# Optimization experiments

Hardware: AMD Instinct MI355X
Metric: run time of the kernel (lower is better)

The kernel has to match this reference:

```python
import jax, jax.numpy as jnp
import numpy as np

VOCAB = 9
D = 128      # EMBED_DIM
S = 64       # SEQ_LEN / context_length
B = 512      # batch
NH = 4       # num_heads
DH = D // NH # head dim = 32
NB = 2       # num_blocks
EPS = 1e-5


def setup_inputs() -> dict:
    key = jax.random.key(0)
    ks = jax.random.split(key, 10)
    rn = lambda k, shape: jax.random.normal(k, shape, jnp.float32) * 0.02
    return {
        "x": jax.random.randint(ks[0], (B, S), 0, VOCAB),
        "emb": rn(ks[1], (VOCAB, D)),
        "ln1_w": jnp.ones((NB, D), jnp.float32),          # pre-sLSTM LayerNorm weight
        "Wg": rn(ks[2], (NB, 4, NH, DH, DH)),             # headwise gate projections (i,f,z,o)
        "R": rn(ks[3], (NB, NH, DH, 4 * DH)),             # recurrent kernels per head
        "bias": rn(ks[4], (NB, NH, 4, DH)),               # cell bias per head/gate
        "gn_w": jnp.ones((NB, D), jnp.float32),           # multi-head (group) norm weight
        "ln2_w": jnp.ones((NB, D), jnp.float32),          # pre-FF LayerNorm weight
        "ff_up_w": rn(ks[5], (NB, 2 * D, D)),             # gated FF up projection
        "ff_down_w": rn(ks[6], (NB, D, D)),               # FF down projection
        "post_w": jnp.ones((D,), jnp.float32),            # post-blocks LayerNorm weight
        "proj_w": rn(ks[7], (VOCAB, D)),
        "proj_b": jnp.zeros((VOCAB,), jnp.float32),
    }


def _layernorm(x, w):
    mu = x.mean(-1, keepdims=True)
    var = x.var(-1, keepdims=True)
    return (x - mu) * jax.lax.rsqrt(var + EPS) * w


def _mh_groupnorm(h, w):
    # h: [B,S,NH,DH] -> normalize over DH per head, scale by per-channel w [D]
    mu = h.mean(-1, keepdims=True)
    var = h.var(-1, keepdims=True)
    hn = (h - mu) * jax.lax.rsqrt(var + EPS)
    return hn.reshape(h.shape[0], h.shape[1], D) * w


def _slstm_layer(xh, Wg, R, b):
    # xh: [B,S,NH,DH]; Wg: [4,NH,DH,DH]; R: [NH,DH,4*DH]; b: [NH,4,DH]
    gx = jnp.einsum('bsnh,gnkh->sbngk', xh, Wg)  # [S,B,NH,4,DH] gate preacts (i,f,z,o)

    def step(carry, g):
        h, c, n, m = carry  # each [B,NH,DH]
        ry = jnp.einsum('bnh,nhk->bnk', h, R).reshape(h.shape[0], NH, 4, DH)
        raw = g + ry + b
        i_r, f_r, z_r, o_r = raw[:, :, 0], raw[:, :, 1], raw[:, :, 2], raw[:, :, 3]
        logfplusm = m + jax.nn.log_sigmoid(f_r)
        mnew = jnp.maximum(i_r, logfplusm)            # stabilizer
        ig = jnp.exp(i_r - mnew)
        fg = jnp.exp(logfplusm - mnew)
        cnew = fg * c + ig * jnp.tanh(z_r)
        nnew = fg * n + ig
        hnew = jax.nn.sigmoid(o_r) * cnew / nnew
        return (hnew, cnew, nnew, mnew), hnew

    z0 = jnp.zeros((xh.shape[0], NH, DH), xh.dtype)
    _, hs = jax.lax.scan(step, (z0, z0, z0, z0), gx)
    return hs.transpose(1, 0, 2, 3)  # [B,S,NH,DH]


def reference(x, emb, ln1_w, Wg, R, bias, gn_w, ln2_w, ff_up_w, ff_down_w, post_w, proj_w, proj_b):
    h = emb[x]  # [B,S,D]
    for bi in range(NB):
        xn = _layernorm(h, ln1_w[bi])
        y = _slstm_layer(xn.reshape(h.shape[0], S, NH, DH), Wg[bi], R[bi], bias[bi])
        h = h + _mh_groupnorm(y, gn_w[bi])
        xn = _layernorm(h, ln2_w[bi])
        up = xn @ ff_up_w[bi].T                       # [B,S,2D]
        gate, upv = up[..., :D], up[..., D:]
        h = h + (jax.nn.gelu(gate, approximate=False) * upv) @ ff_down_w[bi].T
    h = _layernorm(h, post_w)
    return h @ proj_w.T + proj_b  # [B,S,VOCAB]
```

## Files before the change

### kernel.cpp

```cpp
#include <hip/hip_runtime.h>
#include <math.h>

#define D      128
#define S_LEN  64
#define B_SZ   512
#define NH     4
#define DH     32
#define NB     2
#define VOCAB  9
#define EPS    1e-5f
#define NTOK   (B_SZ * S_LEN)

template <int CTRL>
__device__ __forceinline__ float dppf(float x) {
    return __int_as_float(__builtin_amdgcn_update_dpp(
        0, __float_as_int(x), CTRL, 0xF, 0xF, true));
}
__device__ __forceinline__ float wsum64(float x) {
    x += dppf<0x111>(x);
    x += dppf<0x112>(x);
    x += dppf<0x114>(x);
    x += dppf<0x118>(x);
    x += dppf<0x142>(x);
    x += dppf<0x143>(x);
    return __int_as_float(__builtin_amdgcn_readlane(__float_as_int(x), 63));
}

__device__ __forceinline__ int xc3(int t, int c) { return c ^ (((t >> 1) & 7) << 2); }
__device__ __forceinline__ int xa (int t, int c) { return c ^ ((t & 7) << 2); }
__device__ __forceinline__ int xg (int c)        { return c ^ ((c >> 5) << 3); }

__global__ __launch_bounds__(256) void k_embed(const int* __restrict__ x,
                                               const float* __restrict__ emb,
                                               float* __restrict__ h,
                                               float* __restrict__ stats)
{
    int lane = threadIdx.x & 63;
    int wv   = threadIdx.x >> 6;
    int tok  = blockIdx.x * 4 + wv;
    int xi   = x[tok];
    float2 v = ((const float2*)(emb + xi * D))[lane];
    ((float2*)(h + (size_t)tok * D))[lane] = v;
    float s1 = wsum64(v.x + v.y);
    float s2 = wsum64(v.x * v.x + v.y * v.y);
    float mu  = s1 * (1.0f / D);
    float var = s2 * (1.0f / D) - mu * mu;
    if (lane == 0) {
        stats[tok * 2]     = mu;
        stats[tok * 2 + 1] = rsqrtf(var + EPS);
    }
}

__global__ __launch_bounds__(256, 2) void k_gx(const float* __restrict__ Wg,
                                               const float* __restrict__ bias,
                                               const float* __restrict__ lnw,
                                               const float* __restrict__ h,
                                               const float* __restrict__ stats,
                                               float* __restrict__ gx)
{
    __shared__ float xs[32 * 128];
    __shared__ float wl[4 * 32 * 128];

    int tid  = threadIdx.x;
    int lane = tid & 63;
    int wv   = tid >> 6;
    size_t tok0 = (size_t)blockIdx.x * 32;

    {
        int q = tid & 7;
        #pragma unroll
        for (int it = 0; it < 16; ++it) {
            int row = it * 32 + (tid >> 3);
            int g  = row >> 7;
            int n  = (row >> 5) & 3;
            int hh = row & 31;
            float4 v = *(const float4*)(Wg + row * 32 + q * 4);
            int col = g * 32 + hh;
            int sw  = q << 2;
            float* dst = wl + n * 4096;
            dst[(q * 4 + 0) * 128 + (col ^ sw)] = v.x;
            dst[(q * 4 + 1) * 128 + (col ^ sw)] = v.y;
            dst[(q * 4 + 2) * 128 + (col ^ sw)] = v.z;
            dst[(q * 4 + 3) * 128 + (col ^ sw)] = v.w;
        }
    }
    for (int i = 0; i < 8; ++i) {
        int t = wv * 8 + i;
        const float* hp = h + (tok0 + t) * D;
        float mu = stats[(tok0 + t) * 2];
        float rs = stats[(tok0 + t) * 2 + 1];
        float v1 = (hp[lane]      - mu) * rs * lnw[lane];
        float v2 = (hp[64 + lane] - mu) * rs * lnw[64 + lane];
        xs[t * 128 + xg(lane)]      = v1;
        xs[t * 128 + xg(lane + 64)] = v2;
    }
    __syncthreads();

    int nh   = lane >> 4;
    int col0 = (lane & 15) * 8;
    int t0   = wv * 8;

    float acc[8][8];
    #pragma unroll
    for (int j = 0; j < 8; ++j)
        #pragma unroll
        for (int cc = 0; cc < 8; ++cc) acc[j][cc] = 0.f;

    const float* wbase = wl + nh * 4096;
    #pragma unroll
    for (int k4 = 0; k4 < 8; ++k4) {
        int sw  = k4 << 2;
        int ac4 = (nh * 32 + k4 * 4) ^ (nh << 3);
        float4 w0[4], w1[4];
        #pragma unroll
        for (int i = 0; i < 4; ++i) {
            int k = k4 * 4 + i;
            w0[i] = *(const float4*)&wbase[k * 128 + (col0 ^ sw)];
            w1[i] = *(const float4*)&wbase[k * 128 + ((col0 + 4) ^ sw)];
        }
        #pragma unroll
        for (int j = 0; j < 8; ++j) {
            float4 a4 = *(const float4*)&xs[(t0 + j) * 128 + ac4];
            #pragma unroll
            for (int i = 0; i < 4; ++i) {
                float a = ((const float*)&a4)[i];
                acc[j][0] = fmaf(a, w0[i].x, acc[j][0]);
                acc[j][1] = fmaf(a, w0[i].y, acc[j][1]);
                acc[j][2] = fmaf(a, w0[i].z, acc[j][2]);
                acc[j][3] = fmaf(a, w0[i].w, acc[j][3]);
                acc[j][4] = fmaf(a, w1[i].x, acc[j][4]);
                acc[j][5] = fmaf(a, w1[i].y, acc[j][5]);
                acc[j][6] = fmaf(a, w1[i].z, acc[j][6]);
                acc[j][7] = fmaf(a, w1[i].w, acc[j][7]);
            }
        }
    }

    float4 bb0 = *(const float4*)(bias + nh * 128 + col0);
    float4 bb1 = *(const float4*)(bias + nh * 128 + col0 + 4);
    #pragma unroll
    for (int j = 0; j < 8; ++j) {
        int gt = (int)tok0 + t0 + j;
        int bb = gt >> 6;
        int ss = gt & 63;
        float* op = gx + ((size_t)(bb * NH + nh) * S_LEN + ss) * 128 + col0;
        float4 o0v, o1v;
        o0v.x = acc[j][0] + bb0.x; o0v.y = acc[j][1] + bb0.y;
        o0v.z = acc[j][2] + bb0.z; o0v.w = acc[j][3] + bb0.w;
        o1v.x = acc[j][4] + bb1.x; o1v.y = acc[j][5] + bb1.y;
        o1v.z = acc[j][6] + bb1.z; o1v.w = acc[j][7] + bb1.w;
        *(float4*)op       = o0v;
        *(float4*)(op + 4) = o1v;
    }
}

__global__ __launch_bounds__(64, 2) void k_scan(const float* __restrict__ Rm,
                                                const float* __restrict__ gnw,
                                                const float* __restrict__ gx,
                                                float* __restrict__ h)
{
    __shared__ float WA[8][64][4];
    __shared__ float WB[8][64][4];

    int b    = blockIdx.x >> 2;
    int n    = blockIdx.x & 3;
    int lane = threadIdx.x;
    int e    = lane >> 1;
    int sub  = lane & 1;
    int colA = sub * DH + e;

    #pragma unroll
    for (int cc = 0; cc < 8; ++cc) {
        float4 a, bv;
        #pragma unroll
        for (int j = 0; j < 4; ++j) {
            ((float*)&a)[j]  = Rm[(n * DH + cc * 4 + j) * 128 + colA];
            ((float*)&bv)[j] = Rm[(n * DH + cc * 4 + j) * 128 + 64 + colA];
        }
        *(float4*)WA[cc][lane] = a;
        *(float4*)WB[cc][lane] = bv;
    }
    float gw = gnw[n * DH + e];
    __syncthreads();

    float c = 0.f, nacc = 0.f, m = 0.f;
    float hu[DH];
    #pragma unroll
    for (int i = 0; i < DH; ++i) hu[i] = 0.f;

    float* hb = h + ((size_t)b * S_LEN) * D + n * DH;
    const float* gxp = gx + ((size_t)(b * NH + n) * S_LEN) * 128;

    float pGA[4], pGB[4], pHR[4];
    #pragma unroll
    for (int k = 0; k < 4; ++k) {
        pGA[k] = gxp[k * 128 + colA];
        pGB[k] = gxp[k * 128 + 64 + colA];
        pHR[k] = hb[k * D + e];
    }

    #pragma unroll 4
    for (int s = 0; s < S_LEN; ++s) {
        int sp = (s + 4 < S_LEN) ? s + 4 : S_LEN - 1;
        float nGA = gxp[sp * 128 + colA];
        float nGB = gxp[sp * 128 + 64 + colA];
        float nHR = hb[sp * D + e];

        float r0=0,r1=0,r2=0,r3=0,q0=0,q1=0,q2=0,q3=0;
        #pragma unroll
        for (int cc = 0; cc < 8; ++cc) {
            float4 wa = *(const float4*)WA[cc][lane];
            float4 wb = *(const float4*)WB[cc][lane];
            r0 = fmaf(hu[cc*4+0], wa.x, r0);
            r1 = fmaf(hu[cc*4+1], wa.y, r1);
            r2 = fmaf(hu[cc*4+2], wa.z, r2);
            r3 = fmaf(hu[cc*4+3], wa.w, r3);
            q0 = fmaf(hu[cc*4+0], wb.x, q0);
            q1 = fmaf(hu[cc*4+1], wb.y, q1);
            q2 = fmaf(hu[cc*4+2], wb.z, q2);
            q3 = fmaf(hu[cc*4+3], wb.w, q3);
        }
        float rawA = pGA[0] + ((r0 + r1) + (r2 + r3));
        float rawB = pGB[0] + ((q0 + q1) + (q2 + q3));

        float xA = dppf<0xB1>(rawA);
        float xB = dppf<0xB1>(rawB);
        float i_r = sub ? xA   : rawA;
        float f_r = sub ? rawA : xA;
        float z_r = sub ? xB   : rawB;
        float o_r = sub ? rawB : xB;

        float lsf  = fminf(f_r, 0.f)
                   - 0.69314718055994531f * __log2f(1.0f + __expf(-fabsf(f_r)));
        float lfm  = m + lsf;
        float mnew = fmaxf(i_r, lfm);
        float ig   = __expf(i_r - mnew);
        float fg   = __expf(lfm - mnew);
        float t    = __expf(2.f * z_r);
        float tz   = 1.f - 2.f / (t + 1.f);
        c    = fg * c + ig * tz;
        nacc = fg * nacc + ig;
        m    = mnew;
        float hv = c / (nacc * (1.f + __expf(-o_r)));

        float s1 = wsum64(hv);
        float s2 = wsum64(hv * hv);
        float mu  = s1 * (1.f / 64.f);
        float var = s2 * (1.f / 64.f) - mu * mu;
        float hn  = (hv - mu) * rsqrtf(var + EPS) * gw;

        if (!sub) hb[s * D + e] = pHR[0] + hn;

        #pragma unroll
        for (int i = 0; i < DH; ++i)
            hu[i] = __int_as_float(
                __builtin_amdgcn_readlane(__float_as_int(hv), 2 * i));

        pGA[0]=pGA[1]; pGA[1]=pGA[2]; pGA[2]=pGA[3]; pGA[3]=nGA;
        pGB[0]=pGB[1]; pGB[1]=pGB[2]; pGB[2]=pGB[3]; pGB[3]=nGB;
        pHR[0]=pHR[1]; pHR[1]=pHR[2]; pHR[2]=pHR[3]; pHR[3]=nHR;
    }
}

template <int LAST>
__global__ __launch_bounds__(256, 3) void k_ff(float* __restrict__ h,
                                               const float* __restrict__ ln2w,
                                               const float* __restrict__ wup,
                                               const float* __restrict__ wdn,
                                               float* __restrict__ stats_out,
                                               const float* __restrict__ lastw,
                                               const float* __restrict__ projw,
                                               const float* __restrict__ projb,
                                               float* __restrict__ out)
{
    __shared__ float xs[32 * 128];
    __shared__ float as_[32 * 64];
    __shared__ float wt[2 * 32 * 64];

    int tid  = threadIdx.x;
    int lane = tid & 63;
    int wv   = tid >> 6;
    size_t tok0 = (size_t)blockIdx.x * 32;

    for (int i = 0; i < 8; ++i) {
        int t = wv * 8 + i;
        const float* hp = h + (tok0 + t) * D;
        float v1 = hp[lane], v2 = hp[64 + lane];
        float s1 = wsum64(v1 + v2);
        float s2 = wsum64(v1 * v1 + v2 * v2);
        float mu = s1 * (1.0f / D);
        float rs = rsqrtf(s2 * (1.0f / D) - mu * mu + EPS);
        xs[t * D + xc3(t, lane)]      = (v1 - mu) * rs * ln2w[lane];
        xs[t * D + xc3(t, lane + 64)] = (v2 - mu) * rs * ln2w[64 + lane];
    }

    int q     = tid & 7;
    int r0    = tid >> 3;
    int goff0 = r0 * D + q * 4;
    int goff1 = (r0 + 32) * D + q * 4;
    int s0    = r0 ^ (q << 2);
    int kb    = q * 4;

    auto ffld = [&](int id, float4* pre) {
        int p = (id >= 6) ? 1 : 0;
        int j = id - p * 6;
        const float* b0;
        const float* b1;
        if (j < 4) { b0 = wup + (p * 64) * D + j * 32;
                     b1 = wup + (128 + p * 64) * D + j * 32; }
        else       { int jj = j - 4;
                     b0 = wdn + p * 64 + jj * 32;
                     b1 = wdn + 64 * D + p * 64 + jj * 32; }
        pre[0] = *(const float4*)(b0 + goff0);
        pre[1] = *(const float4*)(b0 + goff1);
        pre[2] = *(const float4*)(b1 + goff0);
        pre[3] = *(const float4*)(b1 + goff1);
    };
    auto fst = [&](const float4* pre) {
        #pragma unroll
        for (int cc = 0; cc < 4; ++cc) {
            const float* p0 = (const float*)&pre[0];
            const float* p1 = (const float*)&pre[1];
            const float* p2 = (const float*)&pre[2];
            const float* p3 = (const float*)&pre[3];
            wt[(kb + cc) * 64 + s0]           = p0[cc];
            wt[(kb + cc) * 64 + s0 + 32]      = p1[cc];
            wt[2048 + (kb + cc) * 64 + s0]      = p2[cc];
            wt[2048 + (kb + cc) * 64 + s0 + 32] = p3[cc];
        }
    };

    int ti = tid >> 4;
    int oi = tid & 15;
    int t0 = ti * 2;
    int o0 = oi * 4;

    float accd[2][2][4];
    #pragma unroll
    for (int a1 = 0; a1 < 2; ++a1)
        #pragma unroll
        for (int j = 0; j < 2; ++j)
            #pragma unroll
            for (int cc = 0; cc < 4; ++cc) accd[a1][j][cc] = 0.f;

    float4 pre[4];
    ffld(0, pre);
    int id = 1;

    #pragma unroll
    for (int p = 0; p < 2; ++p) {
        float accg[2][4], accv[2][4];
        #pragma unroll
        for (int j = 0; j < 2; ++j)
            #pragma unroll
            for (int cc = 0; cc < 4; ++cc) { accg[j][cc] = 0.f; accv[j][cc] = 0.f; }

        for (int c4 = 0; c4 < 4; ++c4) {
            __syncthreads();
            fst(pre);
            if (id < 12) ffld(id, pre);
            ++id;
            __syncthreads();
            int kc = c4 * 32;
            #pragma unroll
            for (int k4 = 0; k4 < 8; ++k4) {
                float4 a0 = *(const float4*)&xs[t0 * D + xc3(t0, kc + k4 * 4)];
                float4 a1v = *(const float4*)&xs[(t0 + 1) * D + xc3(t0 + 1, kc + k4 * 4)];
                int ws = k4 << 2;
                #pragma unroll
                for (int i = 0; i < 4; ++i) {
                    int k = k4 * 4 + i;
                    float4 bg = *(const float4*)&wt[k * 64 + (o0 ^ ws)];
                    float4 bv = *(const float4*)&wt[2048 + k * 64 + (o0 ^ ws)];
                    float ax0 = ((const float*)&a0)[i];
                    float ax1 = ((const float*)&a1v)[i];
                    accg[0][0] = fmaf(ax0, bg.x, accg[0][0]);
                    accg[0][1] = fmaf(ax0, bg.y, accg[0][1]);
                    accg[0][2] = fmaf(ax0, bg.z, accg[0][2]);
                    accg[0][3] = fmaf(ax0, bg.w, accg[0][3]);
                    accg[1][0] = fmaf(ax1, bg.x, accg[1][0]);
                    accg[1][1] = fmaf(ax1, bg.y, accg[1][1]);
                    accg[1][2] = fmaf(ax1, bg.z, accg[1][2]);
                    accg[1][3] = fmaf(ax1, bg.w, accg[1][3]);
                    accv[0][0] = fmaf(ax0, bv.x, accv[0][0]);
                    accv[0][1] = fmaf(ax0, bv.y, accv[0][1]);
                    accv[0][2] = fmaf(ax0, bv.z, accv[0][2]);
                    accv[0][3] = fmaf(ax0, bv.w, accv[0][3]);
                    accv[1][0] = fmaf(ax1, bv.x, accv[1][0]);
                    accv[1][1] = fmaf(ax1, bv.y, accv[1][1]);
                    accv[1][2] = fmaf(ax1, bv.z, accv[1][2]);
                    accv[1][3] = fmaf(ax1, bv.w, accv[1][3]);
                }
            }
        }
        #pragma unroll
        for (int j = 0; j < 2; ++j) {
            int t = t0 + j;
            float4 av;
            float* ap = (float*)&av;
            #pragma unroll
            for (int cc = 0; cc < 4; ++cc) {
                float g = accg[j][cc];
                float u = accv[j][cc];
                ap[cc] = 0.5f * g * (1.0f + erff(g * 0.70710678118654752f)) * u;
            }
            *(float4*)&as_[t * 64 + xa(t, o0)] = av;
        }
        for (int c2 = 0; c2 < 2; ++c2) {
            __syncthreads();
            fst(pre);
            if (id < 12) ffld(id, pre);
            ++id;
            __syncthreads();
            int kc = c2 * 32;
            #pragma unroll
            for (int k4 = 0; k4 < 8; ++k4) {
                float4 a0 = *(const float4*)&as_[t0 * 64 + xa(t0, kc + k4 * 4)];
                float4 a1v = *(const float4*)&as_[(t0 + 1) * 64 + xa(t0 + 1, kc + k4 * 4)];
                int ws = k4 << 2;
                #pragma unroll
                for (int i = 0; i < 4; ++i) {
                    int k = k4 * 4 + i;
                    float4 b0v = *(const float4*)&wt[k * 64 + (o0 ^ ws)];
                    float4 b1v = *(const float4*)&wt[2048 + k * 64 + (o0 ^ ws)];
                    float ax0 = ((const float*)&a0)[i];
                    float ax1 = ((const float*)&a1v)[i];
                    accd[0][0][0] = fmaf(ax0, b0v.x, accd[0][0][0]);
                    accd[0][0][1] = fmaf(ax0, b0v.y, accd[0][0][1]);
                    accd[0][0][2] = fmaf(ax0, b0v.z, accd[0][0][2]);
                    accd[0][0][3] = fmaf(ax0, b0v.w, accd[0][0][3]);
                    accd[0][1][0] = fmaf(ax1, b0v.x, accd[0][1][0]);
                    accd[0][1][1] = fmaf(ax1, b0v.y, accd[0][1][1]);
                    accd[0][1][2] = fmaf(ax1, b0v.z, accd[0][1][2]);
                    accd[0][1][3] = fmaf(ax1, b0v.w, accd[0][1][3]);
                    accd[1][0][0] = fmaf(ax0, b1v.x, accd[1][0][0]);
                    accd[1][0][1] = fmaf(ax0, b1v.y, accd[1][0][1]);
                    accd[1][0][2] = fmaf(ax0, b1v.z, accd[1][0][2]);
                    accd[1][0][3] = fmaf(ax0, b1v.w, accd[1][0][3]);
                    accd[1][1][0] = fmaf(ax1, b1v.x, accd[1][1][0]);
                    accd[1][1][1] = fmaf(ax1, b1v.y, accd[1][1][1]);
                    accd[1][1][2] = fmaf(ax1, b1v.z, accd[1][1][2]);
                    accd[1][1][3] = fmaf(ax1, b1v.w, accd[1][1][3]);
                }
            }
        }
    }

    #pragma unroll
    for (int j = 0; j < 2; ++j) {
        int t = t0 + j;
        size_t tok = tok0 + t;
        #pragma unroll
        for (int a1 = 0; a1 < 2; ++a1) {
            int cb = a1 * 64 + o0;
            float4 hres = *(const float4*)(h + tok * D + cb);
            float4 hn;
            hn.x = hres.x + accd[a1][j][0];
            hn.y = hres.y + accd[a1][j][1];
            hn.z = hres.z + accd[a1][j][2];
            hn.w = hres.w + accd[a1][j][3];
            if (!LAST) *(float4*)(h + tok * D + cb) = hn;
            *(float4*)&xs[t * D + xc3(t, cb)] = hn;
        }
    }
    __syncthreads();

    if (!LAST) {
        for (int i = 0; i < 8; ++i) {
            int t = wv * 8 + i;
            float v1 = xs[t * D + xc3(t, lane)];
            float v2 = xs[t * D + xc3(t, lane + 64)];
            float s1 = wsum64(v1 + v2);
            float s2 = wsum64(v1 * v1 + v2 * v2);
            float mu = s1 * (1.0f / D);
            float rs = rsqrtf(s2 * (1.0f / D) - mu * mu + EPS);
            if (lane == 0) {
                stats_out[(tok0 + t) * 2]     = mu;
                stats_out[(tok0 + t) * 2 + 1] = rs;
            }
        }
    } else {
        float pw1[VOCAB], pw2[VOCAB], pb[VOCAB];
        #pragma unroll
        for (int v = 0; v < VOCAB; ++v) {
            pw1[v] = projw[v * D + lane];
            pw2[v] = projw[v * D + 64 + lane];
            pb[v]  = projb[v];
        }
        for (int i = 0; i < 8; ++i) {
            int t = wv * 8 + i;
            float v1 = xs[t * D + xc3(t, lane)];
            float v2 = xs[t * D + xc3(t, lane + 64)];
            float s1 = wsum64(v1 + v2);
            float s2 = wsum64(v1 * v1 + v2 * v2);
            float mu = s1 * (1.0f / D);
            float rs = rsqrtf(s2 * (1.0f / D) - mu * mu + EPS);
            float x1 = (v1 - mu) * rs * lastw[lane];
            float x2 = (v2 - mu) * rs * lastw[64 + lane];
            #pragma unroll
            for (int v = 0; v < VOCAB; ++v) {
                float pp = wsum64(fmaf(x1, pw1[v], x2 * pw2[v]));
                if (lane == 0) out[(tok0 + t) * VOCAB + v] = pp + pb[v];
            }
        }
    }
}

extern "C" void kernel_launch(void* const* d_in, const int* in_sizes, int n_in,
                              void* d_out, int out_size, void* d_ws, size_t ws_size,
                              hipStream_t stream)
{
    const int*   x     = (const int*)  d_in[0];
    const float* emb   = (const float*)d_in[1];
    const float* ln1   = (const float*)d_in[2];
    const float* Wg    = (const float*)d_in[3];
    const float* Rm    = (const float*)d_in[4];
    const float* bias  = (const float*)d_in[5];
    const float* gnw   = (const float*)d_in[6];
    const float* ln2   = (const float*)d_in[7];
    const float* wup   = (const float*)d_in[8];
    const float* wdn   = (const float*)d_in[9];
    const float* postw = (const float*)d_in[10];
    const float* projw = (const float*)d_in[11];
    const float* projb = (const float*)d_in[12];
    float* out   = (float*)d_out;
    float* hbuf  = (float*)d_ws;
    float* stats = hbuf + (size_t)NTOK * D;
    float* gxbuf = stats + (size_t)NTOK * 2;

    k_embed<<<NTOK / 4, 256, 0, stream>>>(x, emb, hbuf, stats);

    for (int bi = 0; bi < NB; ++bi) {
        k_gx<<<NTOK / 32, 256, 0, stream>>>(Wg + bi * 4 * NH * DH * DH,
                                            bias + bi * NH * 4 * DH,
                                            ln1 + bi * D,
                                            hbuf, stats, gxbuf);
        k_scan<<<B_SZ * NH, 64, 0, stream>>>(Rm + bi * NH * DH * 4 * DH,
                                             gnw + bi * D,
                                             gxbuf, hbuf);
        if (bi == 0)
            k_ff<0><<<NTOK / 32, 256, 0, stream>>>(hbuf, ln2 + bi * D,
                                                   wup + bi * 2 * D * D,
                                                   wdn + bi * D * D,
                                                   stats, nullptr, nullptr,
                                                   nullptr, nullptr);
        else
            k_ff<1><<<NTOK / 32, 256, 0, stream>>>(hbuf, ln2 + bi * D,
                                                   wup + bi * 2 * D * D,
                                                   wdn + bi * D * D,
                                                   nullptr, postw, projw,
                                                   projb, out);
    }
}
```

Before: 390.3 us.

## Restructure sLSTM scan: one block per batch, register weights, chunked LDS prefetch

The scan kernel now launches one 256-thread block per batch element, with one wave per head, in place of one 64-thread block per (batch, head). The recurrent weights are copied to LDS once and then held in registers, so the inner dot product no longer reads LDS every step. Gate preactivations and residual inputs are staged in 16-step chunks into double-buffered LDS with coalesced float4 global loads, replacing per-step scalar prefetches. The costs are higher register pressure (64 weight floats plus 32 h values per lane), a large LDS footprint that limits occupancy, and block-wide barriers between chunks.

```diff
diff --git a/kernel.cpp b/kernel.cpp
--- a/kernel.cpp
+++ b/kernel.cpp
@@ -154,111 +154,137 @@
     }
 }
 
-__global__ __launch_bounds__(64, 2) void k_scan(const float* __restrict__ Rm,
-                                                const float* __restrict__ gnw,
-                                                const float* __restrict__ gx,
-                                                float* __restrict__ h)
+__global__ __launch_bounds__(256, 1) void k_scan(const float* __restrict__ Rm,
+                                                 const float* __restrict__ gnw,
+                                                 const float* __restrict__ gx,
+                                                 float* __restrict__ h)
 {
-    __shared__ float WA[8][64][4];
-    __shared__ float WB[8][64][4];
-
-    int b    = blockIdx.x >> 2;
-    int n    = blockIdx.x & 3;
-    int lane = threadIdx.x;
+    __shared__ float lds[20480];
+
+    int tid  = threadIdx.x;
+    int n    = tid >> 6;
+    int lane = tid & 63;
     int e    = lane >> 1;
     int sub  = lane & 1;
     int colA = sub * DH + e;
-
-    #pragma unroll
-    for (int cc = 0; cc < 8; ++cc) {
-        float4 a, bv;
-        #pragma unroll
-        for (int j = 0; j < 4; ++j) {
-            ((float*)&a)[j]  = Rm[(n * DH + cc * 4 + j) * 128 + colA];
-            ((float*)&bv)[j] = Rm[(n * DH + cc * 4 + j) * 128 + 64 + colA];
-        }
-        *(float4*)WA[cc][lane] = a;
-        *(float4*)WB[cc][lane] = bv;
+    int b    = blockIdx.x;
+
+    {
+        const float4* src = (const float4*)Rm;
+        #pragma unroll
+        for (int it = 0; it < 16; ++it) {
+            int f4 = it * 256 + tid;
+            *(float4*)&lds[f4 * 4] = src[f4];
+        }
+    }
+    __syncthreads();
+    float RA[DH], RB[DH];
+    #pragma unroll
+    for (int i = 0; i < DH; ++i) {
+        RA[i] = lds[(n * DH + i) * 128 + colA];
+        RB[i] = lds[(n * DH + i) * 128 + 64 + colA];
     }
     float gw = gnw[n * DH + e];
     __syncthreads();
 
-    float c = 0.f, nacc = 0.f, m = 0.f;
+    const float* gxp = gx + ((size_t)(b * NH + n) * S_LEN) * 128;
+    const float* hbr = h + (size_t)b * S_LEN * D;
+    float*       hbw = h + (size_t)b * S_LEN * D + n * DH;
+
+    float4 gxr[8], hr2[2];
+    auto ld_chunk = [&](int c) {
+        const float* p = gxp + c * 2048;
+        #pragma unroll
+        for (int k = 0; k < 8; ++k)
+            gxr[k] = *(const float4*)(p + (k * 64 + lane) * 4);
+        const float* q = hbr + c * 2048;
+        #pragma unroll
+        for (int k = 0; k < 2; ++k)
+            hr2[k] = *(const float4*)(q + (k * 256 + tid) * 4);
+    };
+    auto st_chunk = [&](int buf) {
+        float* g = lds + buf * 8192 + n * 2048;
+        #pragma unroll
+        for (int k = 0; k < 8; ++k)
+            *(float4*)&g[(k * 64 + lane) * 4] = gxr[k];
+        float* hh = lds + 16384 + buf * 2048;
+        #pragma unroll
+        for (int k = 0; k < 2; ++k)
+            *(float4*)&hh[(k * 256 + tid) * 4] = hr2[k];
+    };
+
+    ld_chunk(0); st_chunk(0); ld_chunk(1);
+    __syncthreads();
+
+    float c_ = 0.f, nacc = 0.f, m = 0.f;
     float hu[DH];
     #pragma unroll
     for (int i = 0; i < DH; ++i) hu[i] = 0.f;
 
-    float* hb = h + ((size_t)b * S_LEN) * D + n * DH;
-    const float* gxp = gx + ((size_t)(b * NH + n) * S_LEN) * 128;
-
-    float pGA[4], pGB[4], pHR[4];
-    #pragma unroll
-    for (int k = 0; k < 4; ++k) {
-        pGA[k] = gxp[k * 128 + colA];
-        pGB[k] = gxp[k * 128 + 64 + colA];
-        pHR[k] = hb[k * D + e];
-    }
-
-    #pragma unroll 4
-    for (int s = 0; s < S_LEN; ++s) {
-        int sp = (s + 4 < S_LEN) ? s + 4 : S_LEN - 1;
-        float nGA = gxp[sp * 128 + colA];
-        float nGB = gxp[sp * 128 + 64 + colA];
-        float nHR = hb[sp * D + e];
-
-        float r0=0,r1=0,r2=0,r3=0,q0=0,q1=0,q2=0,q3=0;
-        #pragma unroll
-        for (int cc = 0; cc < 8; ++cc) {
-            float4 wa = *(const float4*)WA[cc][lane];
-            float4 wb = *(const float4*)WB[cc][lane];
-            r0 = fmaf(hu[cc*4+0], wa.x, r0);
-            r1 = fmaf(hu[cc*4+1], wa.y, r1);
-            r2 = fmaf(hu[cc*4+2], wa.z, r2);
-            r3 = fmaf(hu[cc*4+3], wa.w, r3);
-            q0 = fmaf(hu[cc*4+0], wb.x, q0);
-            q1 = fmaf(hu[cc*4+1], wb.y, q1);
-            q2 = fmaf(hu[cc*4+2], wb.z, q2);
-            q3 = fmaf(hu[cc*4+3], wb.w, q3);
-        }
-        float rawA = pGA[0] + ((r0 + r1) + (r2 + r3));
-        float rawB = pGB[0] + ((q0 + q1) + (q2 + q3));
-
-        float xA = dppf<0xB1>(rawA);
-        float xB = dppf<0xB1>(rawB);
-        float i_r = sub ? xA   : rawA;
-        float f_r = sub ? rawA : xA;
-        float z_r = sub ? xB   : rawB;
-        float o_r = sub ? rawB : xB;
-
-        float lsf  = fminf(f_r, 0.f)
-                   - 0.69314718055994531f * __log2f(1.0f + __expf(-fabsf(f_r)));
-        float lfm  = m + lsf;
-        float mnew = fmaxf(i_r, lfm);
-        float ig   = __expf(i_r - mnew);
-        float fg   = __expf(lfm - mnew);
-        float t    = __expf(2.f * z_r);
-        float tz   = 1.f - 2.f / (t + 1.f);
-        c    = fg * c + ig * tz;
-        nacc = fg * nacc + ig;
-        m    = mnew;
-        float hv = c / (nacc * (1.f + __expf(-o_r)));
-
-        float s1 = wsum64(hv);
-        float s2 = wsum64(hv * hv);
-        float mu  = s1 * (1.f / 64.f);
-        float var = s2 * (1.f / 64.f) - mu * mu;
-        float hn  = (hv - mu) * rsqrtf(var + EPS) * gw;
-
-        if (!sub) hb[s * D + e] = pHR[0] + hn;
-
-        #pragma unroll
-        for (int i = 0; i < DH; ++i)
-            hu[i] = __int_as_float(
-                __builtin_amdgcn_readlane(__float_as_int(hv), 2 * i));
-
-        pGA[0]=pGA[1]; pGA[1]=pGA[2]; pGA[2]=pGA[3]; pGA[3]=nGA;
-        pGB[0]=pGB[1]; pGB[1]=pGB[2]; pGB[2]=pGB[3]; pGB[3]=nGB;
-        pHR[0]=pHR[1]; pHR[1]=pHR[2]; pHR[2]=pHR[3]; pHR[3]=nHR;
+    for (int c = 0; c < 4; ++c) {
+        int buf = c & 1;
+        const float* g  = lds + buf * 8192 + n * 2048;
+        const float* hh = lds + 16384 + buf * 2048;
+
+        for (int i = 0; i < 16; ++i) {
+            float gA   = g[i * 128 + colA];
+            float gB   = g[i * 128 + 64 + colA];
+            float hres = hh[i * 128 + n * 32 + e];
+
+            float r0=0,r1=0,r2=0,r3=0,q0=0,q1=0,q2=0,q3=0;
+            #pragma unroll
+            for (int k = 0; k < DH; k += 4) {
+                r0 = fmaf(hu[k],   RA[k],   r0);
+                r1 = fmaf(hu[k+1], RA[k+1], r1);
+                r2 = fmaf(hu[k+2], RA[k+2], r2);
+                r3 = fmaf(hu[k+3], RA[k+3], r3);
+                q0 = fmaf(hu[k],   RB[k],   q0);
+                q1 = fmaf(hu[k+1], RB[k+1], q1);
+                q2 = fmaf(hu[k+2], RB[k+2], q2);
+                q3 = fmaf(hu[k+3], RB[k+3], q3);
+            }
+            float rawA = gA + ((r0 + r1) + (r2 + r3));
+            float rawB = gB + ((q0 + q1) + (q2 + q3));
+
+            float xA = dppf<0xB1>(rawA);
+            float xB = dppf<0xB1>(rawB);
+            float i_r = sub ? xA   : rawA;
+            float f_r = sub ? rawA : xA;
+            float z_r = sub ? xB   : rawB;
+            float o_r = sub ? rawB : xB;
+
+            float lsf  = fminf(f_r, 0.f)
+                       - 0.69314718055994531f * __log2f(1.0f + __expf(-fabsf(f_r)));
+            float lfm  = m + lsf;
+            float mnew = fmaxf(i_r, lfm);
+            float ig   = __expf(i_r - mnew);
+            float fg   = __expf(lfm - mnew);
+            float t    = __expf(2.f * z_r);
+            float tz   = 1.f - 2.f / (t + 1.f);
+            c_   = fg * c_ + ig * tz;
+            nacc = fg * nacc + ig;
+            m    = mnew;
+            float hv = c_ / (nacc * (1.f + __expf(-o_r)));
+
+            float s1 = wsum64(hv);
+            float s2 = wsum64(hv * hv);
+            float mu  = s1 * (1.f / 64.f);
+            float var = s2 * (1.f / 64.f) - mu * mu;
+            float hn  = (hv - mu) * rsqrtf(var + EPS) * gw;
+
+            if (!sub) hbw[(c * 16 + i) * D + e] = hres + hn;
+
+            #pragma unroll
+            for (int k = 0; k < DH; ++k)
+                hu[k] = __int_as_float(
+                    __builtin_amdgcn_readlane(__float_as_int(hv), 2 * k));
+        }
+
+        if (c < 3) {
+            st_chunk((c + 1) & 1);
+            if (c < 2) ld_chunk(c + 2);
+            __syncthreads();
+        }
     }
 }
 
@@ -535,9 +561,9 @@
                                             bias + bi * NH * 4 * DH,
                                             ln1 + bi * D,
                                             hbuf, stats, gxbuf);
-        k_scan<<<B_SZ * NH, 64, 0, stream>>>(Rm + bi * NH * DH * 4 * DH,
-                                             gnw + bi * D,
-                                             gxbuf, hbuf);
+        k_scan<<<B_SZ, 256, 0, stream>>>(Rm + bi * NH * DH * 4 * DH,
+                                         gnw + bi * D,
+                                         gxbuf, hbuf);
         if (bi == 0)
             k_ff<0><<<NTOK / 32, 256, 0, stream>>>(hbuf, ln2 + bi * D,
                                                    wup + bi * 2 * D * D,
```

Measured after the change: 397.8 us. About the same (+1.9%).
